# Kernel optimization log

Measured on AMD Instinct MI355X. Metric: run time of the kernel, lower is better.

## Reference

```python
import jax, jax.numpy as jnp
import numpy as np

EPS = 1e-5
NUM_HEADS = 8
SPLIT = 7


def _ln(x, g, b):
    mu = jnp.mean(x, -1, keepdims=True)
    var = jnp.mean((x - mu) ** 2, -1, keepdims=True)
    return (x - mu) / jnp.sqrt(var + EPS) * g + b


def _lepe_attn(q, k, v, H, W, H_sp, W_sp, num_heads, conv_w, conv_b):
    # q,k,v: [B, H*W, C] (one branch, C = dim//2)
    B, L, C = q.shape
    d = C // num_heads
    scale = d ** -0.5
    nH, nW = H // H_sp, W // W_sp

    def to_win(t):  # [B,L,C] -> [B*nH*nW, heads, H_sp*W_sp, d]
        t = t.reshape(B, nH, H_sp, nW, W_sp, C).transpose(0, 1, 3, 2, 4, 5)
        return t.reshape(-1, H_sp * W_sp, num_heads, d).transpose(0, 2, 1, 3)

    qw, kw = to_win(q), to_win(k)

    # LePE: depthwise 3x3 conv on v inside each window (get_lepe)
    vimg = v.reshape(B, nH, H_sp, nW, W_sp, C).transpose(0, 1, 3, 2, 4, 5)
    vimg = vimg.reshape(-1, H_sp, W_sp, C)  # [nWin, H_sp, W_sp, C]
    lepe = jax.lax.conv_general_dilated(
        vimg, conv_w, (1, 1), 'SAME',
        dimension_numbers=('NHWC', 'HWIO', 'NHWC'),
        feature_group_count=C) + conv_b

    def img2heads(t):  # [nWin,H_sp,W_sp,C] -> [nWin, heads, N, d]
        return t.reshape(-1, H_sp * W_sp, num_heads, d).transpose(0, 2, 1, 3)

    vw = img2heads(vimg)
    lepe = img2heads(lepe)

    attn = jax.nn.softmax(jnp.einsum('whqd,whkd->whqk', qw * scale, kw), axis=-1)
    out = jnp.einsum('whqk,whkd->whqd', attn, vw) + lepe  # [nWin, heads, N, d]

    # windows2img
    out = out.transpose(0, 2, 1, 3).reshape(B, nH, nW, H_sp, W_sp, C)
    out = out.transpose(0, 1, 3, 2, 4, 5).reshape(B, H * W, C)
    return out


def setup_inputs() -> dict:
    key = jax.random.key(0)
    ks = jax.random.split(key, 12)
    B, H, W, C = 8, 56, 56, 256
    hid = 4 * C
    Cb = C // 2  # per-branch channels
    s = 0.02
    return {
        'x': jax.random.normal(ks[0], (B, H * W, C), jnp.float32),
        'H': H,
        'W': W,
        'norm1_g': jnp.ones((C,), jnp.float32),
        'norm1_b': jnp.zeros((C,), jnp.float32),
        'qkv_w': jax.random.normal(ks[1], (C, 3 * C), jnp.float32) * s,
        'proj_w': jax.random.normal(ks[2], (C, C), jnp.float32) * s,
        'proj_b': jnp.zeros((C,), jnp.float32),
        'conv0_w': jax.random.normal(ks[3], (3, 3, 1, Cb), jnp.float32) * s,
        'conv0_b': jnp.zeros((Cb,), jnp.float32),
        'conv1_w': jax.random.normal(ks[4], (3, 3, 1, Cb), jnp.float32) * s,
        'conv1_b': jnp.zeros((Cb,), jnp.float32),
        'norm2_g': jnp.ones((C,), jnp.float32),
        'norm2_b': jnp.zeros((C,), jnp.float32),
        'fc1_w': jax.random.normal(ks[5], (C, hid), jnp.float32) * s,
        'fc1_b': jnp.zeros((hid,), jnp.float32),
        'fc2_w': jax.random.normal(ks[6], (hid, C), jnp.float32) * s,
        'fc2_b': jnp.zeros((C,), jnp.float32),
    }


def reference(x, H, W, norm1_g, norm1_b, qkv_w, proj_w, proj_b,
              conv0_w, conv0_b, conv1_w, conv1_b,
              norm2_g, norm2_b, fc1_w, fc1_b, fc2_w, fc2_b):
    B, L, C = x.shape
    img = _ln(x, norm1_g, norm1_b)
    qkv = (img @ qkv_w).reshape(B, L, 3, C).transpose(2, 0, 1, 3)  # [3,B,L,C]
    h = C // 2
    # branch 0 (idx=0): full-height stripes; branch 1 (idx=1): full-width stripes
    x1 = _lepe_attn(qkv[0, :, :, :h], qkv[1, :, :, :h], qkv[2, :, :, :h],
                    H, W, H, SPLIT, NUM_HEADS // 2, conv0_w, conv0_b)
    x2 = _lepe_attn(qkv[0, :, :, h:], qkv[1, :, :, h:], qkv[2, :, :, h:],
                    H, W, SPLIT, W, NUM_HEADS // 2, conv1_w, conv1_b)
    att = jnp.concatenate([x1, x2], axis=2) @ proj_w + proj_b
    x = x + att
    y = _ln(x, norm2_g, norm2_b)
    y = jax.nn.gelu(y @ fc1_w + fc1_b, approximate=False) @ fc2_w + fc2_b
    return x + y
```

## Files before the change

kernel.cpp:

```cpp
#include <hip/hip_runtime.h>
#include <hip/hip_bf16.h>
#include <math.h>

constexpr int C_DIM = 256;
constexpr int MROWS = 25088;
constexpr int HID   = 1024;

typedef float  f32x4 __attribute__((ext_vector_type(4)));
typedef short  s16x8 __attribute__((ext_vector_type(8)));

__device__ __forceinline__ ushort f2bf(float f) {
    __hip_bfloat16 h = __float2bfloat16(f);
    return *reinterpret_cast<ushort*>(&h);
}
__device__ __forceinline__ unsigned pkbf2(float a, float b) {
    __hip_bfloat162 h = __float22bfloat162_rn(float2{a, b});
    return *reinterpret_cast<unsigned*>(&h);
}
__device__ __forceinline__ float bf2f(ushort u) {
    return __uint_as_float(((unsigned)u) << 16);
}

__device__ __forceinline__ float fast_gelu(float v) {
    float u = v * (0.7978845608028654f + 0.035677408136f * v * v);
    float e = __expf(2.0f * u);
    float t = 1.0f - 2.0f / (e + 1.0f);
    return 0.5f * v * (1.0f + t);
}

typedef const __attribute__((address_space(1))) unsigned guint;
typedef __attribute__((address_space(3))) unsigned luint;
__device__ __forceinline__ void gload16(const void* g, void* l) {
    __builtin_amdgcn_global_load_lds((guint*)g, (luint*)l, 16, 0, 0);
}

__global__ __launch_bounds__(256) void ln_kernel(
    const float* __restrict__ x, const float* __restrict__ g,
    const float* __restrict__ b, ushort* __restrict__ out)
{
    int wv = threadIdx.x >> 6, lane = threadIdx.x & 63;
    size_t row = (size_t)blockIdx.x * 4 + wv;
    float4 v = *(const float4*)(x + row * 256 + lane * 4);
    float s1 = v.x + v.y + v.z + v.w;
    float s2 = v.x*v.x + v.y*v.y + v.z*v.z + v.w*v.w;
    #pragma unroll
    for (int d = 1; d < 64; d <<= 1) {
        s1 += __shfl_xor(s1, d);
        s2 += __shfl_xor(s2, d);
    }
    float mu  = s1 * (1.0f / 256.0f);
    float var = s2 * (1.0f / 256.0f) - mu * mu;
    float inv = rsqrtf(var + 1e-5f);
    float4 gv = *(const float4*)(g + lane * 4);
    float4 bv = *(const float4*)(b + lane * 4);
    uint2 o;
    o.x = pkbf2((v.x - mu) * inv * gv.x + bv.x, (v.y - mu) * inv * gv.y + bv.y);
    o.y = pkbf2((v.z - mu) * inv * gv.z + bv.z, (v.w - mu) * inv * gv.w + bv.w);
    *(uint2*)(out + row * 256 + lane * 4) = o;
}

__global__ __launch_bounds__(256) void wcvt_all(
    const float* __restrict__ w0, const float* __restrict__ w1,
    const float* __restrict__ w2, const float* __restrict__ w3,
    ushort* __restrict__ o0, ushort* __restrict__ o1,
    ushort* __restrict__ o2, ushort* __restrict__ o3)
{
    __shared__ ushort tile[64][65];
    int bid = blockIdx.x;
    const float* w; ushort* o; int K, N, tIdx;
    if (bid < 48)       { w = w0; o = o0; K = 256;  N = 768;  tIdx = bid; }
    else if (bid < 64)  { w = w1; o = o1; K = 256;  N = 256;  tIdx = bid - 48; }
    else if (bid < 128) { w = w2; o = o2; K = 256;  N = 1024; tIdx = bid - 64; }
    else                { w = w3; o = o3; K = 1024; N = 256;  tIdx = bid - 128; }
    int nx = N >> 6;
    int bx = tIdx % nx, by = tIdx / nx;
    int n0 = bx * 64, k0 = by * 64;
    int c = threadIdx.x & 63, rr = threadIdx.x >> 6;
    #pragma unroll
    for (int i = 0; i < 64; i += 4) {
        int r = i + rr;
        tile[r][c] = f2bf(w[(size_t)(k0 + r) * N + n0 + c]);
    }
    __syncthreads();
    #pragma unroll
    for (int i = 0; i < 64; i += 4) {
        int r = i + rr;
        o[(size_t)(n0 + r) * K + k0 + c] = tile[c][r];
    }
}

template<int FUSE>
__global__ __launch_bounds__(256) void gemm_bf16(
    const ushort* __restrict__ A, const ushort* __restrict__ Bt,
    const float* __restrict__ bias, const float* res,
    void* Cout, int M, int N, int K, int NBX)
{
    __shared__ ushort As[2][128 * 32];
    __shared__ ushort Bs[2][128 * 32];
    int tid  = threadIdx.x;
    int lane = tid & 63, wv = tid >> 6;
    int lr = lane & 15, lg = lane >> 4;

    int nwg = gridDim.x;
    int qc = nwg >> 3, rc = nwg & 7;
    int xcd = blockIdx.x & 7, pos = blockIdx.x >> 3;
    int wg = (xcd < rc ? xcd * (qc + 1) : rc * (qc + 1) + (xcd - rc) * qc) + pos;
    int row0 = (wg / NBX) * 128, col0 = (wg % NBX) * 128;
    int wr = wv >> 1, wc = wv & 1;

    f32x4 acc[4][4];
    #pragma unroll
    for (int n = 0; n < 4; ++n)
        #pragma unroll
        for (int m = 0; m < 4; ++m)
            acc[n][m] = (f32x4){0.f, 0.f, 0.f, 0.f};

    int srow = wv * 32 + (lane >> 2);
    const ushort* gA  = A  + (size_t)(row0 + srow) * K + (lane & 3) * 8;
    const ushort* gA2 = gA + (size_t)16 * K;
    const ushort* gB  = Bt + (size_t)(col0 + srow) * K + (lane & 3) * 8;
    const ushort* gB2 = gB + (size_t)16 * K;

#define STAGE(buf, k0) do {                                      \
        gload16(gA  + (k0), &As[buf][(wv * 32 +  0) * 32]);      \
        gload16(gA2 + (k0), &As[buf][(wv * 32 + 16) * 32]);      \
        gload16(gB  + (k0), &Bs[buf][(wv * 32 +  0) * 32]);      \
        gload16(gB2 + (k0), &Bs[buf][(wv * 32 + 16) * 32]);      \
    } while (0)

#define COMPUTE(buf) do {                                                          \
        s16x8 af[4], bfg[4];                                                       \
        _Pragma("unroll")                                                          \
        for (int m = 0; m < 4; ++m)                                                \
            af[m] = *(const s16x8*)&As[buf][(wr * 64 + m * 16 + lr) * 32 + lg * 8];\
        _Pragma("unroll")                                                          \
        for (int n = 0; n < 4; ++n)                                                \
            bfg[n] = *(const s16x8*)&Bs[buf][(wc * 64 + n * 16 + lr) * 32 + lg * 8];\
        _Pragma("unroll")                                                          \
        for (int n = 0; n < 4; ++n)                                                \
            _Pragma("unroll")                                                      \
            for (int m = 0; m < 4; ++m)                                            \
                acc[n][m] = __builtin_amdgcn_mfma_f32_16x16x32_bf16(               \
                    bfg[n], af[m], acc[n][m], 0, 0, 0);                            \
    } while (0)

    STAGE(0, 0);
    __syncthreads();
    #pragma unroll 1
    for (int k0 = 0; k0 + 64 <= K; k0 += 64) {
        STAGE(1, k0 + 32);
        COMPUTE(0);
        __syncthreads();
        if (k0 + 64 < K) STAGE(0, k0 + 64);
        COMPUTE(1);
        __syncthreads();
    }
#undef STAGE
#undef COMPUTE

    int grow0 = row0 + wr * 64;
    int gcol0 = col0 + wc * 64;
    #pragma unroll
    for (int n = 0; n < 4; ++n) {
        int gcol = gcol0 + n * 16 + lg * 4;
        float4 b4 = make_float4(0.f, 0.f, 0.f, 0.f);
        if (FUSE >= 1) b4 = *(const float4*)&bias[gcol];
        #pragma unroll
        for (int m = 0; m < 4; ++m) {
            int grow = grow0 + m * 16 + lr;
            float v0 = acc[n][m][0] + b4.x;
            float v1 = acc[n][m][1] + b4.y;
            float v2 = acc[n][m][2] + b4.z;
            float v3 = acc[n][m][3] + b4.w;
            if (FUSE == 2) {
                v0 = fast_gelu(v0); v1 = fast_gelu(v1);
                v2 = fast_gelu(v2); v3 = fast_gelu(v3);
            }
            if (FUSE == 1) {
                const float4 rr = *(const float4*)&res[(size_t)grow * N + gcol];
                float4 o = make_float4(v0 + rr.x, v1 + rr.y, v2 + rr.z, v3 + rr.w);
                *(float4*)&((float*)Cout)[(size_t)grow * N + gcol] = o;
            } else {
                uint2 o;
                o.x = pkbf2(v0, v1);
                o.y = pkbf2(v2, v3);
                *(uint2*)&((ushort*)Cout)[(size_t)grow * N + gcol] = o;
            }
        }
    }
}

__device__ __forceinline__ int wrow(int branch, int b, int wi, int n) {
    if (branch) return b * 3136 + wi * 392 + n;
    int ii = n / 7;
    return b * 3136 + ii * 56 + wi * 7 + (n - ii * 7);
}

__global__ __launch_bounds__(512, 2) void attn_kernel(
    const ushort* __restrict__ qkv,
    const float* __restrict__ c0w, const float* __restrict__ c0b,
    const float* __restrict__ c1w, const float* __restrict__ c1b,
    ushort* __restrict__ att)
{
    __shared__ ushort Kh[2 * 416 * 16];
    __shared__ ushort Vt[32][424];
    __shared__ ushort Pl[8][16][40];
    __shared__ float  CwS[9][32];
    __shared__ float  CbS[32];

    int bid    = blockIdx.x;
    int branch = bid >> 8;
    int rem    = bid & 255;
    int head   = rem & 3;
    int win    = rem >> 2;
    int b  = win >> 3, wi = win & 7;
    int c0 = branch * 128 + head * 32;
    const float* cw = branch ? c1w : c0w;
    const float* cb = branch ? c1b : c0b;
    int tid = threadIdx.x;

    if (tid < 288) {
        int tap = tid >> 5, d = tid & 31;
        CwS[tap][d] = cw[tap * 128 + head * 32 + d];
    } else if (tid < 320) {
        CbS[tid - 288] = cb[head * 32 + (tid - 288)];
    }
    for (int e = tid; e < 1664; e += 512) {
        int n = e >> 2, quad = e & 3;
        uint4 v = make_uint4(0u, 0u, 0u, 0u);
        if (n < 392) {
            int gr = wrow(branch, b, wi, n);
            v = *(const uint4*)(qkv + (size_t)gr * 768 + 256 + c0 + quad * 8);
        }
        *(uint4*)&Kh[(quad >> 1) * 6656 + n * 16 + (quad & 1) * 8] = v;
    }
    for (int e = tid; e < 1568; e += 512) {
        int n = e >> 2, quad = e & 3;
        int gr = wrow(branch, b, wi, n);
        uint4 v = *(const uint4*)(qkv + (size_t)gr * 768 + 512 + c0 + quad * 8);
        const ushort* us = (const ushort*)&v;
        #pragma unroll
        for (int j = 0; j < 8; ++j) Vt[quad * 8 + j][n] = us[j];
    }
    for (int e = tid; e < 1024; e += 512) {
        int d = e >> 5, k = 392 + (e & 31);
        Vt[d][k] = 0;
    }
    __syncthreads();

    int wv = tid >> 6, lane = tid & 63;
    int lr = lane & 15, lg = lane >> 4;
    constexpr float kSc = 0.17677669529663689f * 1.4426950408889634f;
    ushort* Pw = &Pl[wv][0][0];
    int Hsp = branch ? 7 : 56, Wsp = branch ? 56 : 7;
    const ushort* Kbase = &Kh[(lg >> 1) * 6656 + lr * 16 + (lg & 1) * 8];

    for (int qt = wv; qt < 25; qt += 8) {
        int q0 = qt * 16;
        int qn = q0 + lr; if (qn > 391) qn = 391;
        int qr = wrow(branch, b, wi, qn);
        s16x8 qf = *(const s16x8*)(qkv + (size_t)qr * 768 + c0 + lg * 8);

        f32x4 o0 = {0.f, 0.f, 0.f, 0.f}, o1 = {0.f, 0.f, 0.f, 0.f};
        float psum = 0.0f;

        auto do_chunk = [&](int c, bool last) {
            f32x4 z = {0.f, 0.f, 0.f, 0.f};
            s16x8 kf0 = *(const s16x8*)&Kbase[(c * 32)      * 16];
            s16x8 kf1 = *(const s16x8*)&Kbase[(c * 32 + 16) * 16];
            f32x4 s0 = __builtin_amdgcn_mfma_f32_16x16x32_bf16(kf0, qf, z, 0, 0, 0);
            f32x4 s1 = __builtin_amdgcn_mfma_f32_16x16x32_bf16(kf1, qf, z, 0, 0, 0);
            float p[2][4];
            #pragma unroll
            for (int r = 0; r < 4; ++r) {
                p[0][r] = exp2f(s0[r] * kSc);
                p[1][r] = exp2f(s1[r] * kSc);
            }
            if (last) {
                #pragma unroll
                for (int t = 0; t < 2; ++t)
                    #pragma unroll
                    for (int r = 0; r < 4; ++r) {
                        int kk = 384 + t * 16 + lg * 4 + r;
                        if (kk >= 392) p[t][r] = 0.0f;
                    }
            }
            #pragma unroll
            for (int t = 0; t < 2; ++t)
                #pragma unroll
                for (int r = 0; r < 4; ++r) psum += p[t][r];
            uint2 w0, w1;
            w0.x = pkbf2(p[0][0], p[0][1]); w0.y = pkbf2(p[0][2], p[0][3]);
            w1.x = pkbf2(p[1][0], p[1][1]); w1.y = pkbf2(p[1][2], p[1][3]);
            *(uint2*)&Pw[lr * 40 + lg * 4]      = w0;
            *(uint2*)&Pw[lr * 40 + 16 + lg * 4] = w1;
            s16x8 pf = *(const s16x8*)&Pw[lr * 40 + lg * 8];
            s16x8 v0 = *(const s16x8*)&Vt[lr][c * 32 + lg * 8];
            s16x8 v1 = *(const s16x8*)&Vt[16 + lr][c * 32 + lg * 8];
            o0 = __builtin_amdgcn_mfma_f32_16x16x32_bf16(pf, v0, o0, 0, 0, 0);
            o1 = __builtin_amdgcn_mfma_f32_16x16x32_bf16(pf, v1, o1, 0, 0, 0);
        };

        for (int c = 0; c < 12; ++c) do_chunk(c, false);
        do_chunk(12, true);

        psum += __shfl_xor(psum, 16);
        psum += __shfl_xor(psum, 32);
        float linv[4];
        #pragma unroll
        for (int r = 0; r < 4; ++r)
            linv[r] = 1.0f / __shfl(psum, lg * 4 + r);
        #pragma unroll
        for (int r = 0; r < 4; ++r) { o0[r] *= linv[r]; o1[r] *= linv[r]; }

        #pragma unroll
        for (int r = 0; r < 4; ++r) {
            int q = q0 + lg * 4 + r;
            if (q >= 392) continue;
            int ii = branch ? (q / 56) : (q / 7);
            int jj = q - ii * Wsp;
            float a0 = o0[r], a1 = o1[r];
            #pragma unroll
            for (int kh = 0; kh < 3; ++kh) {
                int i2 = ii + kh - 1;
                if ((unsigned)i2 >= (unsigned)Hsp) continue;
                #pragma unroll
                for (int kw = 0; kw < 3; ++kw) {
                    int j2 = jj + kw - 1;
                    if ((unsigned)j2 >= (unsigned)Wsp) continue;
                    int pos = i2 * Wsp + j2;
                    a0 += CwS[kh * 3 + kw][lr]      * bf2f(Vt[lr][pos]);
                    a1 += CwS[kh * 3 + kw][16 + lr] * bf2f(Vt[16 + lr][pos]);
                }
            }
            a0 += CbS[lr]; a1 += CbS[16 + lr];
            int gr = wrow(branch, b, wi, q);
            att[(size_t)gr * 256 + branch * 128 + head * 32 + lr]      = f2bf(a0);
            att[(size_t)gr * 256 + branch * 128 + head * 32 + 16 + lr] = f2bf(a1);
        }
    }
}

extern "C" void kernel_launch(void* const* d_in, const int* in_sizes, int n_in,
                              void* d_out, int out_size, void* d_ws, size_t ws_size,
                              hipStream_t stream)
{
    const float* x      = (const float*)d_in[0];
    const float* n1g    = (const float*)d_in[3];
    const float* n1b    = (const float*)d_in[4];
    const float* qkv_w  = (const float*)d_in[5];
    const float* proj_w = (const float*)d_in[6];
    const float* proj_b = (const float*)d_in[7];
    const float* c0w    = (const float*)d_in[8];
    const float* c0b    = (const float*)d_in[9];
    const float* c1w    = (const float*)d_in[10];
    const float* c1b    = (const float*)d_in[11];
    const float* n2g    = (const float*)d_in[12];
    const float* n2b    = (const float*)d_in[13];
    const float* fc1_w  = (const float*)d_in[14];
    const float* fc1_b  = (const float*)d_in[15];
    const float* fc2_w  = (const float*)d_in[16];
    const float* fc2_b  = (const float*)d_in[17];
    float* out = (float*)d_out;

    char* ws = (char*)d_ws;
    const size_t SZ_BF = (size_t)MROWS * C_DIM * 2;
    ushort* img  = (ushort*)(ws);
    ushort* att  = (ushort*)(ws + SZ_BF);
    ushort* big  = (ushort*)(ws + 2 * SZ_BF);
    char*   wbase = ws + 2 * SZ_BF + (size_t)MROWS * HID * 2;
    ushort* qkvT = (ushort*)(wbase);
    ushort* projT= (ushort*)(wbase +  393216);
    ushort* fc1T = (ushort*)(wbase +  393216 + 131072);
    ushort* fc2T = (ushort*)(wbase +  393216 + 131072 + 524288);

    wcvt_all<<<192, 256, 0, stream>>>(qkv_w, proj_w, fc1_w, fc2_w, qkvT, projT, fc1T, fc2T);

    ln_kernel<<<MROWS / 4, 256, 0, stream>>>(x, n1g, n1b, img);
    gemm_bf16<0><<<196 * 6, 256, 0, stream>>>(
        img, qkvT, nullptr, nullptr, big, MROWS, 768, 256, 6);
    attn_kernel<<<512, 512, 0, stream>>>(big, c0w, c0b, c1w, c1b, att);
    gemm_bf16<1><<<196 * 2, 256, 0, stream>>>(
        att, projT, proj_b, x, out, MROWS, 256, 256, 2);
    ln_kernel<<<MROWS / 4, 256, 0, stream>>>(out, n2g, n2b, img);
    gemm_bf16<2><<<196 * 8, 256, 0, stream>>>(
        img, fc1T, fc1_b, nullptr, big, MROWS, HID, 256, 8);
    gemm_bf16<1><<<196 * 2, 256, 0, stream>>>(
        big, fc2T, fc2_b, out, out, MROWS, 256, 1024, 2);
}
```

Measured before the change: 312.6 us.

## Triple-buffer GEMM pipeline and move attention P exchange into registers

The GEMM moves from two LDS buffers to three, prefetching two k-steps ahead. It uses a single waitcnt+barrier per step instead of two syncthreads per 64-wide step. The attention kernel drops the LDS round-trip for the softmax P tile and rebuilds the MFMA operand with cross-lane shuffles. It also XOR-swizzles the K layout to reduce bank conflicts, skips the second QK MFMA on the final partial chunk, and raises wave priority around MFMAs. This trades more LDS in the GEMM (possible occupancy loss) and extra shuffle instructions for fewer barriers and less LDS traffic.

```diff
diff --git a/kernel.cpp b/kernel.cpp
--- a/kernel.cpp
+++ b/kernel.cpp
@@ -95,8 +95,8 @@
     const float* __restrict__ bias, const float* res,
     void* Cout, int M, int N, int K, int NBX)
 {
-    __shared__ ushort As[2][128 * 32];
-    __shared__ ushort Bs[2][128 * 32];
+    __shared__ __align__(16) ushort As[3][128 * 32];
+    __shared__ __align__(16) ushort Bs[3][128 * 32];
     int tid  = threadIdx.x;
     int lane = tid & 63, wv = tid >> 6;
     int lr = lane & 15, lg = lane >> 4;
@@ -121,42 +121,41 @@
     const ushort* gB  = Bt + (size_t)(col0 + srow) * K + (lane & 3) * 8;
     const ushort* gB2 = gB + (size_t)16 * K;
 
-#define STAGE(buf, k0) do {                                      \
-        gload16(gA  + (k0), &As[buf][(wv * 32 +  0) * 32]);      \
-        gload16(gA2 + (k0), &As[buf][(wv * 32 + 16) * 32]);      \
-        gload16(gB  + (k0), &Bs[buf][(wv * 32 +  0) * 32]);      \
-        gload16(gB2 + (k0), &Bs[buf][(wv * 32 + 16) * 32]);      \
-    } while (0)
-
-#define COMPUTE(buf) do {                                                          \
-        s16x8 af[4], bfg[4];                                                       \
-        _Pragma("unroll")                                                          \
-        for (int m = 0; m < 4; ++m)                                                \
-            af[m] = *(const s16x8*)&As[buf][(wr * 64 + m * 16 + lr) * 32 + lg * 8];\
-        _Pragma("unroll")                                                          \
-        for (int n = 0; n < 4; ++n)                                                \
-            bfg[n] = *(const s16x8*)&Bs[buf][(wc * 64 + n * 16 + lr) * 32 + lg * 8];\
-        _Pragma("unroll")                                                          \
-        for (int n = 0; n < 4; ++n)                                                \
-            _Pragma("unroll")                                                      \
-            for (int m = 0; m < 4; ++m)                                            \
-                acc[n][m] = __builtin_amdgcn_mfma_f32_16x16x32_bf16(               \
-                    bfg[n], af[m], acc[n][m], 0, 0, 0);                            \
-    } while (0)
-
-    STAGE(0, 0);
-    __syncthreads();
-    #pragma unroll 1
-    for (int k0 = 0; k0 + 64 <= K; k0 += 64) {
-        STAGE(1, k0 + 32);
-        COMPUTE(0);
-        __syncthreads();
-        if (k0 + 64 < K) STAGE(0, k0 + 64);
-        COMPUTE(1);
-        __syncthreads();
-    }
-#undef STAGE
-#undef COMPUTE
+    auto stage = [&](int buf, int k0) {
+        gload16(gA  + k0, &As[buf][(wv * 32 +  0) * 32]);
+        gload16(gA2 + k0, &As[buf][(wv * 32 + 16) * 32]);
+        gload16(gB  + k0, &Bs[buf][(wv * 32 +  0) * 32]);
+        gload16(gB2 + k0, &Bs[buf][(wv * 32 + 16) * 32]);
+    };
+
+    const int NSTEP = K >> 5;
+    stage(0, 0);
+    stage(1, 32);
+    asm volatile("s_waitcnt vmcnt(4)\n\ts_barrier" ::: "memory");
+
+    for (int i = 0; i < NSTEP; ++i) {
+        int cur = i % 3;
+        const ushort* as = As[cur];
+        const ushort* bs = Bs[cur];
+        s16x8 af[4], bfg[4];
+        #pragma unroll
+        for (int m = 0; m < 4; ++m)
+            af[m] = *(const s16x8*)&as[(wr * 64 + m * 16 + lr) * 32 + lg * 8];
+        #pragma unroll
+        for (int n = 0; n < 4; ++n)
+            bfg[n] = *(const s16x8*)&bs[(wc * 64 + n * 16 + lr) * 32 + lg * 8];
+        if (i + 2 < NSTEP) stage((i + 2) % 3, (i + 2) * 32);
+        #pragma unroll
+        for (int n = 0; n < 4; ++n)
+            #pragma unroll
+            for (int m = 0; m < 4; ++m)
+                acc[n][m] = __builtin_amdgcn_mfma_f32_16x16x32_bf16(
+                    bfg[n], af[m], acc[n][m], 0, 0, 0);
+        if (i + 2 < NSTEP)
+            asm volatile("s_waitcnt vmcnt(4)\n\ts_barrier" ::: "memory");
+        else if (i + 1 < NSTEP)
+            asm volatile("s_waitcnt vmcnt(0)\n\ts_barrier" ::: "memory");
+    }
 
     int grow0 = row0 + wr * 64;
     int gcol0 = col0 + wc * 64;
@@ -202,9 +201,8 @@
     const float* __restrict__ c1w, const float* __restrict__ c1b,
     ushort* __restrict__ att)
 {
-    __shared__ ushort Kh[2 * 416 * 16];
-    __shared__ ushort Vt[32][424];
-    __shared__ ushort Pl[8][16][40];
+    __shared__ __align__(16) ushort Kh[2 * 400 * 16];
+    __shared__ __align__(16) ushort Vt[32][424];
     __shared__ float  CwS[9][32];
     __shared__ float  CbS[32];
 
@@ -225,14 +223,15 @@
     } else if (tid < 320) {
         CbS[tid - 288] = cb[head * 32 + (tid - 288)];
     }
-    for (int e = tid; e < 1664; e += 512) {
+    for (int e = tid; e < 1600; e += 512) {
         int n = e >> 2, quad = e & 3;
         uint4 v = make_uint4(0u, 0u, 0u, 0u);
         if (n < 392) {
             int gr = wrow(branch, b, wi, n);
             v = *(const uint4*)(qkv + (size_t)gr * 768 + 256 + c0 + quad * 8);
         }
-        *(uint4*)&Kh[(quad >> 1) * 6656 + n * 16 + (quad & 1) * 8] = v;
+        int idx = ((quad >> 1) * 6400 + n * 16 + (quad & 1) * 8) ^ (((n >> 2) & 1) << 3);
+        *(uint4*)&Kh[idx] = v;
     }
     for (int e = tid; e < 1568; e += 512) {
         int n = e >> 2, quad = e & 3;
@@ -251,9 +250,12 @@
     int wv = tid >> 6, lane = tid & 63;
     int lr = lane & 15, lg = lane >> 4;
     constexpr float kSc = 0.17677669529663689f * 1.4426950408889634f;
-    ushort* Pw = &Pl[wv][0][0];
     int Hsp = branch ? 7 : 56, Wsp = branch ? 56 : 7;
-    const ushort* Kbase = &Kh[(lg >> 1) * 6656 + lr * 16 + (lg & 1) * 8];
+    int kidx = (((lg >> 1) * 6400) + lr * 16 + (lg & 1) * 8) ^ (((lr >> 2) & 1) << 3);
+    const ushort* Kbase = &Kh[kidx];
+    int sA = lr + ((2 * lg) & 3) * 16;
+    int sB = lr + ((2 * lg + 1) & 3) * 16;
+    bool loP = (lg < 2);
 
     for (int qt = wv; qt < 25; qt += 8) {
         int q0 = qt * 16;
@@ -266,39 +268,44 @@
 
         auto do_chunk = [&](int c, bool last) {
             f32x4 z = {0.f, 0.f, 0.f, 0.f};
-            s16x8 kf0 = *(const s16x8*)&Kbase[(c * 32)      * 16];
-            s16x8 kf1 = *(const s16x8*)&Kbase[(c * 32 + 16) * 16];
+            s16x8 kf0 = *(const s16x8*)&Kbase[c * 512];
+            __builtin_amdgcn_s_setprio(1);
             f32x4 s0 = __builtin_amdgcn_mfma_f32_16x16x32_bf16(kf0, qf, z, 0, 0, 0);
-            f32x4 s1 = __builtin_amdgcn_mfma_f32_16x16x32_bf16(kf1, qf, z, 0, 0, 0);
-            float p[2][4];
+            f32x4 s1 = z;
+            if (!last) {
+                s16x8 kf1 = *(const s16x8*)&Kbase[c * 512 + 256];
+                s1 = __builtin_amdgcn_mfma_f32_16x16x32_bf16(kf1, qf, z, 0, 0, 0);
+            }
+            __builtin_amdgcn_s_setprio(0);
+            float p0[4], p1[4];
             #pragma unroll
             for (int r = 0; r < 4; ++r) {
-                p[0][r] = exp2f(s0[r] * kSc);
-                p[1][r] = exp2f(s1[r] * kSc);
-            }
-            if (last) {
+                p0[r] = exp2f(s0[r] * kSc);
+                p1[r] = last ? 0.0f : exp2f(s1[r] * kSc);
+            }
+            if (last && !loP) {
                 #pragma unroll
-                for (int t = 0; t < 2; ++t)
-                    #pragma unroll
-                    for (int r = 0; r < 4; ++r) {
-                        int kk = 384 + t * 16 + lg * 4 + r;
-                        if (kk >= 392) p[t][r] = 0.0f;
-                    }
+                for (int r = 0; r < 4; ++r) p0[r] = 0.0f;
             }
             #pragma unroll
-            for (int t = 0; t < 2; ++t)
-                #pragma unroll
-                for (int r = 0; r < 4; ++r) psum += p[t][r];
-            uint2 w0, w1;
-            w0.x = pkbf2(p[0][0], p[0][1]); w0.y = pkbf2(p[0][2], p[0][3]);
-            w1.x = pkbf2(p[1][0], p[1][1]); w1.y = pkbf2(p[1][2], p[1][3]);
-            *(uint2*)&Pw[lr * 40 + lg * 4]      = w0;
-            *(uint2*)&Pw[lr * 40 + 16 + lg * 4] = w1;
-            s16x8 pf = *(const s16x8*)&Pw[lr * 40 + lg * 8];
+            for (int r = 0; r < 4; ++r) psum += p0[r] + p1[r];
+            unsigned A0 = pkbf2(p0[0], p0[1]), A1 = pkbf2(p0[2], p0[3]);
+            unsigned B0 = pkbf2(p1[0], p1[1]), B1 = pkbf2(p1[2], p1[3]);
+            unsigned a0A = __shfl(A0, sA), a1A = __shfl(A1, sA);
+            unsigned b0A = __shfl(B0, sA), b1A = __shfl(B1, sA);
+            unsigned a0B = __shfl(A0, sB), a1B = __shfl(A1, sB);
+            unsigned b0B = __shfl(B0, sB), b1B = __shfl(B1, sB);
+            union { unsigned u[4]; s16x8 v; } pu;
+            pu.u[0] = loP ? a0A : b0A;
+            pu.u[1] = loP ? a1A : b1A;
+            pu.u[2] = loP ? a0B : b0B;
+            pu.u[3] = loP ? a1B : b1B;
             s16x8 v0 = *(const s16x8*)&Vt[lr][c * 32 + lg * 8];
             s16x8 v1 = *(const s16x8*)&Vt[16 + lr][c * 32 + lg * 8];
-            o0 = __builtin_amdgcn_mfma_f32_16x16x32_bf16(pf, v0, o0, 0, 0, 0);
-            o1 = __builtin_amdgcn_mfma_f32_16x16x32_bf16(pf, v1, o1, 0, 0, 0);
+            __builtin_amdgcn_s_setprio(1);
+            o0 = __builtin_amdgcn_mfma_f32_16x16x32_bf16(pu.v, v0, o0, 0, 0, 0);
+            o1 = __builtin_amdgcn_mfma_f32_16x16x32_bf16(pu.v, v1, o1, 0, 0, 0);
+            __builtin_amdgcn_s_setprio(0);
         };
 
         for (int c = 0; c < 12; ++c) do_chunk(c, false);
```

Measured after the change: 274.0 us. 12.3% less time.
